# Kernel optimization log

Hardware: AMD Instinct MI355X
Metric: run time of the kernel (lower is better)

The kernel has to match this reference:

```python
import jax, jax.numpy as jnp
import numpy as np
from jax import lax

B, C, H, W = 4, 128, 64, 64
D = C // 2          # VSSBlock hidden_dim
DI = 2 * D          # SS2D d_inner (expand=2)
N = 16              # d_state
R = max(D // 16, 1) # dt_rank
K = 4               # scan directions

def dwconv(x, w, b):
    y = lax.conv_general_dilated(x, w, (1, 1), [(1, 1), (1, 1)],
        dimension_numbers=('NCHW', 'OIHW', 'NCHW'), feature_group_count=x.shape[1])
    return y + b[None, :, None, None]

def layer_norm(x, g, b, eps=1e-5):
    mu = jnp.mean(x, axis=-1, keepdims=True)
    var = jnp.var(x, axis=-1, keepdims=True)
    return (x - mu) * lax.rsqrt(var + eps) * g + b

def selective_scan(u, delta, A, Bs, Cs, Dp):
    # u, delta: (B,K,DI,L); Bs, Cs: (B,K,N,L); A: (K,DI,N); Dp: (K,DI)
    uT = jnp.moveaxis(u, -1, 0)
    dT = jnp.moveaxis(delta, -1, 0)
    BT = jnp.moveaxis(Bs, -1, 0)
    CT = jnp.moveaxis(Cs, -1, 0)
    h0 = jnp.zeros(u.shape[:3] + (A.shape[-1],), u.dtype)
    def step(h, inp):
        u_t, d_t, B_t, C_t = inp
        dA = jnp.exp(d_t[..., None] * A)                       # (B,K,DI,N)
        h = dA * h + (d_t * u_t)[..., None] * B_t[:, :, None, :]
        return h, jnp.einsum('bkdn,bkn->bkd', h, C_t)
    _, ys = lax.scan(step, h0, (uT, dT, BT, CT))
    return jnp.moveaxis(ys, 0, -1) + Dp[None, :, :, None] * u  # (B,K,DI,L)

def ss2d(x, in_proj_w, conv_w, conv_b, x_proj_w, dt_w, dt_b, A_logs, Ds, on_g, on_b, out_proj_w):
    # x: (B,H,W,D)
    b, h, w, _ = x.shape
    L = h * w
    xz = x @ in_proj_w.T                                       # (B,H,W,2*DI)
    xc, z = jnp.split(xz, 2, axis=-1)
    xc = jnp.transpose(xc, (0, 3, 1, 2))                       # (B,DI,H,W)
    xc = jax.nn.silu(dwconv(xc, conv_w, conv_b))
    x1 = xc.reshape(b, DI, L)                                  # row-major scan
    x2 = jnp.transpose(xc, (0, 1, 3, 2)).reshape(b, DI, L)     # col-major scan
    xs = jnp.stack([x1, x2, x1[:, :, ::-1], x2[:, :, ::-1]], axis=1)  # (B,K,DI,L)
    x_dbl = jnp.einsum('bkdl,kcd->bkcl', xs, x_proj_w)
    dts, Bsx, Csx = jnp.split(x_dbl, [R, R + N], axis=2)
    delta = jax.nn.softplus(jnp.einsum('bkrl,kdr->bkdl', dts, dt_w) + dt_b[None, :, :, None])
    A = -jnp.exp(A_logs).reshape(K, DI, N)
    out_y = selective_scan(xs, delta, A, Bsx, Csx, Ds.reshape(K, DI))  # (B,K,DI,L)
    inv_y = out_y[:, 2:4, :, ::-1]
    wh_y = jnp.transpose(out_y[:, 1].reshape(b, DI, w, h), (0, 1, 3, 2)).reshape(b, DI, L)
    invwh_y = jnp.transpose(inv_y[:, 1].reshape(b, DI, w, h), (0, 1, 3, 2)).reshape(b, DI, L)
    y = out_y[:, 0] + inv_y[:, 0] + wh_y + invwh_y             # (B,DI,L)
    y = jnp.transpose(y, (0, 2, 1)).reshape(b, h, w, DI)
    y = layer_norm(y, on_g, on_b) * jax.nn.silu(z)
    return y @ out_proj_w.T                                    # (B,H,W,D)

def _forward(x, dw_w, dw_b, scale, ln1_g, ln1_b, in_proj_w, conv_w, conv_b, x_proj_w, dt_w, dt_b, A_logs, Ds, out_norm_g, out_norm_b, out_proj_w, in_gamma, in_beta):
    xd = dwconv(x, dw_w, dw_b)
    x_1, x_2 = jnp.split(xd, 2, axis=1)
    def branch(xi):
        xp = jnp.transpose(xi, (0, 2, 3, 1))                   # (B,H,W,D)
        y = xp + ss2d(layer_norm(xp, ln1_g, ln1_b), in_proj_w, conv_w, conv_b,
                      x_proj_w, dt_w, dt_b, A_logs, Ds, out_norm_g, out_norm_b, out_proj_w)
        return scale * xi + jnp.transpose(y, (0, 3, 1, 2))
    xo = jnp.concatenate([branch(x_1), branch(x_2)], axis=1)
    mu = jnp.mean(xo, axis=(2, 3), keepdims=True)              # InstanceNorm2d(affine)
    var = jnp.var(xo, axis=(2, 3), keepdims=True)
    xo = (xo - mu) * lax.rsqrt(var + 1e-5) * in_gamma[None, :, None, None] + in_beta[None, :, None, None]
    return jnp.where(xo > 0, xo, 0.01 * xo)                    # LeakyReLU(0.01)

def setup_inputs():
    ks = jax.random.split(jax.random.key(0), 12)
    f = lambda k, shp, s=0.02: jax.random.normal(k, shp, jnp.float32) * s
    return dict(
        x=jax.random.normal(ks[0], (B, C, H, W), jnp.float32),
        dw_w=f(ks[1], (C, 1, 3, 3), 0.1), dw_b=f(ks[2], (C,), 0.1),
        scale=jnp.ones((1,), jnp.float32),
        ln1_g=jnp.ones((D,), jnp.float32), ln1_b=jnp.zeros((D,), jnp.float32),
        in_proj_w=f(ks[3], (2 * DI, D)),
        conv_w=f(ks[4], (DI, 1, 3, 3), 0.1), conv_b=f(ks[5], (DI,), 0.1),
        x_proj_w=f(ks[6], (K, R + 2 * N, DI)),
        dt_w=f(ks[7], (K, DI, R), 0.1), dt_b=f(ks[8], (K, DI), 0.1),
        A_logs=f(ks[9], (K * DI, N), 0.5), Ds=jnp.ones((K * DI,), jnp.float32),
        out_norm_g=jnp.ones((DI,), jnp.float32), out_norm_b=jnp.zeros((DI,), jnp.float32),
        out_proj_w=f(ks[10], (D, DI)),
        in_gamma=jnp.ones((C,), jnp.float32), in_beta=jnp.zeros((C,), jnp.float32),
    )

def reference(x, dw_w, dw_b, scale, ln1_g, ln1_b, in_proj_w, conv_w, conv_b, x_proj_w, dt_w, dt_b, A_logs, Ds, out_norm_g, out_norm_b, out_proj_w, in_gamma, in_beta):
    return _forward(x, dw_w, dw_b, scale, ln1_g, ln1_b, in_proj_w, conv_w, conv_b, x_proj_w, dt_w, dt_b, A_logs, Ds, out_norm_g, out_norm_b, out_proj_w, in_gamma, in_beta)
```

## Files before the change

### kernel.cpp

```cpp
#include <hip/hip_runtime.h>
#include <hip/hip_bf16.h>


__device__ __forceinline__ float LD(const void* p, size_t i, bool isb) {
  if (isb) {
    unsigned short u = ((const unsigned short*)p)[i];
    return __uint_as_float(((unsigned)u) << 16);
  }
  return ((const float*)p)[i];
}
__device__ __forceinline__ unsigned short f2bf(float f) {
  unsigned u = __float_as_uint(f);
  u = (u + 0x7FFFu + ((u >> 16) & 1u)) >> 16;
  return (unsigned short)u;
}
__device__ __forceinline__ float silu_(float x) { return x / (1.f + __expf(-x)); }
__device__ __forceinline__ float softplus_(float x) {
  return x > 20.f ? x : __logf(1.f + __expf(x));
}
#define EXP2R(x) __builtin_amdgcn_exp2f(x)

__global__ void kdet(const void* x, int* flag) {
  if (threadIdx.x == 0 && blockIdx.x == 0) {
    const unsigned short* xs = (const unsigned short*)x;
    int bad = 0;
    for (int i = 0; i < 64; ++i) {
      int e = (xs[2 * i] >> 7) & 0xFF;
      if (e > 150 || e < 100) bad++;
    }
    *flag = (bad >= 16) ? 0 : 1;
  }
}

__global__ __launch_bounds__(256) void k0_conv_ln(
    const void* x, const void* dww, const void* dwb, const void* lg, const void* lb,
    const int* __restrict__ flag,
    float* __restrict__ T1, float* __restrict__ T2)
{
  bool isb = (*flag != 0);
  int e = blockIdx.x >> 6, h = blockIdx.x & 63;
  int b = e & 3, br = e >> 2;
  int t = threadIdx.x;
  __shared__ float sIn[3][64][67];
  for (int idx = t; idx < 3 * 64; idx += 256) {
    int r = idx >> 6, d = idx & 63;
    sIn[r][d][0] = 0.f; sIn[r][d][65] = 0.f;
  }
  for (int idx = t; idx < 3 * 64 * 64; idx += 256) {
    int r = idx >> 12, rem = idx & 4095, d = rem >> 6, w = rem & 63;
    int hh = h + r - 1;
    float v = 0.f;
    if (hh >= 0 && hh < 64) v = LD(x, ((size_t)(b * 128 + br * 64 + d) * 64 + hh) * 64 + w, isb);
    sIn[r][d][1 + w] = v;
  }
  __syncthreads();
  int w = t >> 2, g = t & 3;
  float vals[16]; float psum = 0.f, psq = 0.f;
#pragma unroll
  for (int j = 0; j < 16; ++j) {
    int d = g * 16 + j, c = br * 64 + d;
    float s = LD(dwb, c, isb);
#pragma unroll
    for (int kh = 0; kh < 3; ++kh)
#pragma unroll
      for (int kw = 0; kw < 3; ++kw)
        s += LD(dww, c * 9 + kh * 3 + kw, isb) * sIn[kh][d][w + kw];
    vals[j] = s; psum += s; psq += s * s;
  }
  size_t base = ((size_t)e * 4096 + h * 64) * 64 + (size_t)t * 16;
#pragma unroll
  for (int j4 = 0; j4 < 4; ++j4) {
    float4 o; o.x = vals[j4*4]; o.y = vals[j4*4+1]; o.z = vals[j4*4+2]; o.w = vals[j4*4+3];
    *(float4*)(T1 + base + j4 * 4) = o;
  }
  __shared__ float sS[64][4], sQ[64][4];
  sS[w][g] = psum; sQ[w][g] = psq;
  __syncthreads();
  float m = (sS[w][0] + sS[w][1] + sS[w][2] + sS[w][3]) * (1.f / 64.f);
  float q = (sQ[w][0] + sQ[w][1] + sQ[w][2] + sQ[w][3]) * (1.f / 64.f);
  float rs = rsqrtf(q - m * m + 1e-5f);
#pragma unroll
  for (int j4 = 0; j4 < 4; ++j4) {
    float tmp[4];
#pragma unroll
    for (int jj = 0; jj < 4; ++jj) {
      int j = j4 * 4 + jj; int d = g * 16 + j;
      tmp[jj] = (vals[j] - m) * rs * LD(lg, d, isb) + LD(lb, d, isb);
    }
    float4 o; o.x = tmp[0]; o.y = tmp[1]; o.z = tmp[2]; o.w = tmp[3];
    *(float4*)(T2 + base + j4 * 4) = o;
  }
}

__global__ __launch_bounds__(256) void k2_inproj(
    const float* __restrict__ T2, const void* Wip, const int* __restrict__ flag,
    float* __restrict__ T3, float* __restrict__ T4)
{
  bool isb = (*flag != 0);
  int mt = blockIdx.x, ct = blockIdx.y;
  int t = threadIdx.x;
  __shared__ float sA[64][68];
  __shared__ float sB[64][68];
  int row0 = mt * 64;
  for (int q = t; q < 1024; q += 256) {
    int l = q >> 4, d4 = (q & 15) * 4;
    float4 v = *(const float4*)(T2 + (size_t)(row0 + l) * 64 + d4);
    sA[d4][l] = v.x; sA[d4+1][l] = v.y; sA[d4+2][l] = v.z; sA[d4+3][l] = v.w;
  }
  for (int q = t; q < 1024; q += 256) {
    int cl = q >> 4, d4 = (q & 15) * 4;
    size_t base = (size_t)(ct * 64 + cl) * 64 + d4;
    sB[d4][cl]   = LD(Wip, base, isb);
    sB[d4+1][cl] = LD(Wip, base + 1, isb);
    sB[d4+2][cl] = LD(Wip, base + 2, isb);
    sB[d4+3][cl] = LD(Wip, base + 3, isb);
  }
  __syncthreads();
  int ty = t >> 4, tx = t & 15;
  float acc[4][4];
#pragma unroll
  for (int i = 0; i < 4; ++i)
#pragma unroll
    for (int j = 0; j < 4; ++j) acc[i][j] = 0.f;
  for (int kk = 0; kk < 64; ++kk) {
    float4 a = *(const float4*)&sA[kk][ty * 4];
    float4 bq = *(const float4*)&sB[kk][tx * 4];
    float aa[4] = {a.x, a.y, a.z, a.w}, bb[4] = {bq.x, bq.y, bq.z, bq.w};
#pragma unroll
    for (int i = 0; i < 4; ++i)
#pragma unroll
      for (int j = 0; j < 4; ++j) acc[i][j] += aa[i] * bb[j];
  }
  int c0 = ct * 64 + tx * 4;
#pragma unroll
  for (int i = 0; i < 4; ++i) {
    size_t row = (size_t)row0 + ty * 4 + i;
    float4 o;
    if (c0 < 128) {
      o.x = acc[i][0]; o.y = acc[i][1]; o.z = acc[i][2]; o.w = acc[i][3];
      *(float4*)(T3 + row * 128 + c0) = o;
    } else {
      o.x = silu_(acc[i][0]); o.y = silu_(acc[i][1]); o.z = silu_(acc[i][2]); o.w = silu_(acc[i][3]);
      *(float4*)(T4 + row * 128 + (c0 - 128)) = o;
    }
  }
}

__global__ __launch_bounds__(256) void k3_conv2(
    const float* __restrict__ T3, const void* cw, const void* cb, const void* Ds,
    const int* __restrict__ flag,
    float* __restrict__ U0, float* __restrict__ U1, float* __restrict__ Ysum)
{
  bool isb = (*flag != 0);
  int e = blockIdx.x >> 6, h = blockIdx.x & 63, dc = blockIdx.y;
  int t = threadIdx.x;
  __shared__ float sI[3][66][65];
  for (int idx = t; idx < 3 * 2 * 64; idx += 256) {
    int r = idx / 128, rem = idx % 128, side = rem >> 6, d = rem & 63;
    sI[r][side * 65][d] = 0.f;
  }
  for (int idx = t; idx < 3 * 64 * 64; idx += 256) {
    int r = idx >> 12, rem = idx & 4095, w = rem >> 6, d = rem & 63;
    int hh = h + r - 1;
    float v = 0.f;
    if (hh >= 0 && hh < 64) v = T3[((size_t)e * 4096 + hh * 64 + w) * 128 + dc * 64 + d];
    sI[r][1 + w][d] = v;
  }
  __syncthreads();
  int d = t & 63, wq = t >> 6;
  int c2 = dc * 64 + d;
  float wt[9];
#pragma unroll
  for (int m = 0; m < 9; ++m) wt[m] = LD(cw, c2 * 9 + m, isb);
  float bias = LD(cb, c2, isb);
  float sd = LD(Ds, c2, isb) + LD(Ds, 128 + c2, isb) + LD(Ds, 256 + c2, isb) + LD(Ds, 384 + c2, isb);
  size_t eb = (size_t)e * 4096;
#pragma unroll
  for (int i = 0; i < 16; ++i) {
    int w = wq * 16 + i;
    float s = bias;
#pragma unroll
    for (int kh = 0; kh < 3; ++kh)
#pragma unroll
      for (int kw = 0; kw < 3; ++kw)
        s += wt[kh * 3 + kw] * sI[kh][w + kw][d];
    s = silu_(s);
    U0[(eb + h * 64 + w) * 128 + c2] = s;
    U1[(eb + w * 64 + h) * 128 + c2] = s;
    Ysum[(eb + h * 64 + w) * 128 + c2] = sd * s;
  }
}

__global__ __launch_bounds__(256) void k5_xdbl(
    const float* __restrict__ U0, const float* __restrict__ U1,
    const void* xpw, const int* __restrict__ flag,
    float* __restrict__ dts4, float* __restrict__ Bb2, float* __restrict__ Cb2)
{
  bool isb = (*flag != 0);
  int lt = blockIdx.x;
  int ek = blockIdx.y;
  int e = ek >> 2, k = ek & 3;
  int ls0 = lt * 64;
  int t = threadIdx.x;
  __shared__ float sU[64][132];
  __shared__ float sW[36][132];
  for (int idx = t; idx < 36 * 128; idx += 256) {
    int c = idx >> 7, d = idx & 127;
    sW[c][d] = LD(xpw, ((size_t)k * 36 + c) * 128 + d, isb);
  }
  const float* usrc = (k & 1) ? U1 : U0;
  bool rev = (k >= 2);
  for (int idx = t; idx < 2048; idx += 256) {
    int l = idx >> 5, d4 = (idx & 31) * 4;
    int row = rev ? (4095 - ls0 - l) : (ls0 + l);
    float4 v = *(const float4*)(usrc + ((size_t)e * 4096 + row) * 128 + d4);
    *(float4*)&sU[l][d4] = v;
  }
  __syncthreads();
  int l = t & 63, cg = t >> 6;
  float acc[9];
#pragma unroll
  for (int j = 0; j < 9; ++j) acc[j] = 0.f;
  for (int dd = 0; dd < 32; ++dd) {
    float4 u4 = *(const float4*)&sU[l][dd * 4];
    float ua[4] = {u4.x, u4.y, u4.z, u4.w};
#pragma unroll
    for (int j = 0; j < 9; ++j) {
      float4 w4 = *(const float4*)&sW[cg * 9 + j][dd * 4];
      acc[j] += ua[0] * w4.x + ua[1] * w4.y + ua[2] * w4.z + ua[3] * w4.w;
    }
  }
  size_t row = (size_t)ek * 4096 + ls0 + l;
  if (cg == 0) {
    float4 o; o.x = acc[0]; o.y = acc[1]; o.z = acc[2]; o.w = acc[3];
    *(float4*)(dts4 + row * 4) = o;
#pragma unroll
    for (int j = 4; j < 9; ++j) Bb2[row * 16 + (j - 4)] = acc[j];
  } else {
#pragma unroll
    for (int j = 0; j < 9; ++j) {
      int c = cg * 9 + j;
      if (c < 20) Bb2[row * 16 + (c - 4)] = acc[j];
      else Cb2[row * 16 + (c - 20)] = acc[j];
    }
  }
}

template<int NSTEPS>
__global__ __launch_bounds__(128) void k6a_chunk(
    const float* __restrict__ U0, const float* __restrict__ U1,
    const float* __restrict__ dts4, const float* __restrict__ Bb2,
    const void* alog, const void* dtw, const void* dtb, const int* __restrict__ flag,
    float* __restrict__ Hs)
{
  bool isb = (*flag != 0);
  int chunk = blockIdx.x, ek = blockIdx.y;
  int e = ek >> 2, k = ek & 3;
  int d = threadIdx.x;
  int ls0 = chunk * NSTEPS;
  float a2[16];
#pragma unroll
  for (int n = 0; n < 16; ++n)
    a2[n] = -__expf(LD(alog, ((size_t)k * 128 + d) * 16 + n, isb)) * 1.44269504f;
  float w0 = LD(dtw, ((size_t)k * 128 + d) * 4 + 0, isb);
  float w1 = LD(dtw, ((size_t)k * 128 + d) * 4 + 1, isb);
  float w2 = LD(dtw, ((size_t)k * 128 + d) * 4 + 2, isb);
  float w3 = LD(dtw, ((size_t)k * 128 + d) * 4 + 3, isb);
  float bd = LD(dtb, k * 128 + d, isb);
  float h[16];
#pragma unroll
  for (int n = 0; n < 16; ++n) h[n] = 0.f;
  float sdelta = 0.f;
  const float* usrc = (k & 1) ? U1 : U0;
  const bool rev = (k >= 2);
  const float* ubase = usrc + (size_t)e * 4096 * 128 + d;
  const float4* sbase = (const float4*)(dts4 + ((size_t)ek * 4096 + ls0) * 4);
  const float4* bbase = (const float4*)(Bb2 + ((size_t)ek * 4096 + ls0) * 16);
#pragma unroll 2
  for (int t = 0; t < NSTEPS; ++t) {
    float4 s4 = sbase[t];
    float xv = bd + w0 * s4.x + w1 * s4.y + w2 * s4.z + w3 * s4.w;
    float dlt = softplus_(xv);
    int urow = rev ? (4095 - ls0 - t) : (ls0 + t);
    float uu = ubase[(size_t)urow * 128];
    float du = dlt * uu;
    float4 b0 = bbase[t * 4 + 0], b1 = bbase[t * 4 + 1], b2 = bbase[t * 4 + 2], b3 = bbase[t * 4 + 3];
    float bb[16] = {b0.x,b0.y,b0.z,b0.w, b1.x,b1.y,b1.z,b1.w,
                    b2.x,b2.y,b2.z,b2.w, b3.x,b3.y,b3.z,b3.w};
    sdelta += dlt;
#pragma unroll
    for (int n = 0; n < 16; ++n) {
      float dA = EXP2R(dlt * a2[n]);
      h[n] = fmaf(dA, h[n], du * bb[n]);
    }
  }
  float2* hp = (float2*)Hs + ((size_t)chunk * 65536 + ek * 2048 + d * 16);
#pragma unroll
  for (int n = 0; n < 16; ++n) {
    float2 o; o.x = h[n]; o.y = EXP2R(a2[n] * sdelta);
    hp[n] = o;
  }
}

__global__ __launch_bounds__(256) void k6b_carry(
    float* __restrict__ Hs, int nchunks)
{
  int idx = blockIdx.x * 256 + threadIdx.x;
  float2* hs = (float2*)Hs;
  float carry = 0.f;
  for (int c = 0; c < nchunks; ++c) {
    float2 v = hs[(size_t)c * 65536 + idx];
    Hs[((size_t)c * 65536 + idx) * 2] = carry;
    carry = v.x + v.y * carry;
  }
}

template<int NSTEPS>
__global__ __launch_bounds__(128) void k6c_apply(
    const float* __restrict__ U0, const float* __restrict__ U1,
    float* __restrict__ Ysum, const float* __restrict__ dts4,
    const float* __restrict__ Bb2, const float* __restrict__ Cb2,
    const void* alog, const void* dtw, const void* dtb,
    const float* __restrict__ Hs, const int* __restrict__ flag)
{
  bool isb = (*flag != 0);
  int chunk = blockIdx.x, ek = blockIdx.y;
  int e = ek >> 2, k = ek & 3;
  int d = threadIdx.x;
  int ls0 = chunk * NSTEPS;
  float a2[16];
#pragma unroll
  for (int n = 0; n < 16; ++n)
    a2[n] = -__expf(LD(alog, ((size_t)k * 128 + d) * 16 + n, isb)) * 1.44269504f;
  float w0 = LD(dtw, ((size_t)k * 128 + d) * 4 + 0, isb);
  float w1 = LD(dtw, ((size_t)k * 128 + d) * 4 + 1, isb);
  float w2 = LD(dtw, ((size_t)k * 128 + d) * 4 + 2, isb);
  float w3 = LD(dtw, ((size_t)k * 128 + d) * 4 + 3, isb);
  float bd = LD(dtb, k * 128 + d, isb);
  float h[16];
  const float* hp = Hs + ((size_t)chunk * 65536 + ek * 2048 + d * 16) * 2;
#pragma unroll
  for (int n = 0; n < 16; ++n) h[n] = hp[2 * n];
  const float* usrc = (k & 1) ? U1 : U0;
  const bool rev = (k >= 2);
  float* ybase = Ysum + (size_t)e * 4096 * 128 + d;
  const float* ubase = usrc + (size_t)e * 4096 * 128 + d;
  const float4* sbase = (const float4*)(dts4 + ((size_t)ek * 4096 + ls0) * 4);
  const float4* bbase = (const float4*)(Bb2 + ((size_t)ek * 4096 + ls0) * 16);
  const float4* cbase = (const float4*)(Cb2 + ((size_t)ek * 4096 + ls0) * 16);
#pragma unroll 2
  for (int t = 0; t < NSTEPS; ++t) {
    float4 s4 = sbase[t];
    float xv = bd + w0 * s4.x + w1 * s4.y + w2 * s4.z + w3 * s4.w;
    float dlt = softplus_(xv);
    int urow = rev ? (4095 - ls0 - t) : (ls0 + t);
    float uu = ubase[(size_t)urow * 128];
    float du = dlt * uu;
    float4 b0 = bbase[t * 4 + 0], b1 = bbase[t * 4 + 1], b2 = bbase[t * 4 + 2], b3 = bbase[t * 4 + 3];
    float4 c0 = cbase[t * 4 + 0], c1 = cbase[t * 4 + 1], c2 = cbase[t * 4 + 2], c3 = cbase[t * 4 + 3];
    float bb[16] = {b0.x,b0.y,b0.z,b0.w, b1.x,b1.y,b1.z,b1.w,
                    b2.x,b2.y,b2.z,b2.w, b3.x,b3.y,b3.z,b3.w};
    float cc[16] = {c0.x,c0.y,c0.z,c0.w, c1.x,c1.y,c1.z,c1.w,
                    c2.x,c2.y,c2.z,c2.w, c3.x,c3.y,c3.z,c3.w};
    float ya = 0.f, yb = 0.f, yc = 0.f, yd = 0.f;
#pragma unroll
    for (int n = 0; n < 16; n += 4) {
      float dA0 = EXP2R(dlt * a2[n]);
      float dA1 = EXP2R(dlt * a2[n+1]);
      float dA2 = EXP2R(dlt * a2[n+2]);
      float dA3 = EXP2R(dlt * a2[n+3]);
      h[n]   = fmaf(dA0, h[n],   du * bb[n]);
      h[n+1] = fmaf(dA1, h[n+1], du * bb[n+1]);
      h[n+2] = fmaf(dA2, h[n+2], du * bb[n+2]);
      h[n+3] = fmaf(dA3, h[n+3], du * bb[n+3]);
      ya = fmaf(h[n],   cc[n],   ya);
      yb = fmaf(h[n+1], cc[n+1], yb);
      yc = fmaf(h[n+2], cc[n+2], yc);
      yd = fmaf(h[n+3], cc[n+3], yd);
    }
    int p = ls0 + t;
    int orow;
    if (k == 0)      orow = p;
    else if (k == 1) orow = ((p & 63) << 6) | (p >> 6);
    else if (k == 2) orow = 4095 - p;
    else { int q = 4095 - p; orow = ((q & 63) << 6) | (q >> 6); }
    atomicAdd(ybase + (size_t)orow * 128, (ya + yb) + (yc + yd));
  }
}

__global__ __launch_bounds__(256) void k7b_out(
    const float* __restrict__ Ysum, const float* __restrict__ T4,
    const float* __restrict__ T1,
    const void* ong, const void* onb, const void* opw, const void* scale_p,
    const int* __restrict__ flag,
    float* __restrict__ P)
{
  bool isb = (*flag != 0);
  int bid = blockIdx.x; int e = bid >> 7, lt = bid & 127;
  int l0 = lt * 32;
  int t = threadIdx.x;
  __shared__ float sY[32][132];
  __shared__ float sWo[64][132];
  __shared__ float sMu[32], sRs[32];
  __shared__ float sPs[32][8], sPq[32][8];
  __shared__ float sP[64][33];
  for (int idx = t; idx < 8192; idx += 256) sWo[idx >> 7][idx & 127] = LD(opw, idx, isb);
  for (int q = t; q < 1024; q += 256) {
    int l = q >> 5, d4 = (q & 31) * 4;
    float4 v = *(const float4*)(Ysum + ((size_t)e * 4096 + l0 + l) * 128 + d4);
    *(float4*)&sY[l][d4] = v;
  }
  __syncthreads();
  {
    int l = t & 31, g = t >> 5;
    float s = 0.f, q2 = 0.f;
#pragma unroll
    for (int j = 0; j < 16; ++j) { float v = sY[l][g * 16 + j]; s += v; q2 += v * v; }
    sPs[l][g] = s; sPq[l][g] = q2;
  }
  __syncthreads();
  if (t < 32) {
    float s = 0.f, q2 = 0.f;
#pragma unroll
    for (int g = 0; g < 8; ++g) { s += sPs[t][g]; q2 += sPq[t][g]; }
    float mu = s * (1.f / 128.f);
    float var = q2 * (1.f / 128.f) - mu * mu;
    sMu[t] = mu; sRs[t] = rsqrtf(var + 1e-5f);
  }
  __syncthreads();
  for (int idx = t; idx < 4096; idx += 256) {
    int l = idx >> 7, dd2 = idx & 127;
    float v = (sY[l][dd2] - sMu[l]) * sRs[l] * LD(ong, dd2, isb) + LD(onb, dd2, isb);
    v *= T4[((size_t)e * 4096 + l0 + l) * 128 + dd2];
    sY[l][dd2] = v;
  }
  __syncthreads();
  float ops = 1.f + LD(scale_p, 0, isb);
  {
    int l = t & 31, cg = t >> 5;
    float acc[8];
#pragma unroll
    for (int j = 0; j < 8; ++j) acc[j] = 0.f;
    for (int dd = 0; dd < 32; ++dd) {
      float4 v4 = *(const float4*)&sY[l][dd * 4];
      float va[4] = {v4.x, v4.y, v4.z, v4.w};
#pragma unroll
      for (int j = 0; j < 8; ++j) {
        float4 w4 = *(const float4*)&sWo[cg * 8 + j][dd * 4];
        acc[j] += va[0] * w4.x + va[1] * w4.y + va[2] * w4.z + va[3] * w4.w;
      }
    }
#pragma unroll
    for (int j = 0; j < 8; ++j) {
      int c = cg * 8 + j;
      sP[c][l] = acc[j] + ops * T1[((size_t)e * 4096 + l0 + l) * 64 + c];
    }
  }
  __syncthreads();
  for (int q = t; q < 512; q += 256) {
    int c = q >> 3, lq = (q & 7) * 4;
    float4 o; o.x = sP[c][lq]; o.y = sP[c][lq+1]; o.z = sP[c][lq+2]; o.w = sP[c][lq+3];
    *(float4*)(P + ((size_t)e * 64 + c) * 4096 + l0 + lq) = o;
  }
}

__global__ __launch_bounds__(256) void k7c_final(
    const float* __restrict__ P, const void* gamma, const void* beta,
    const int* __restrict__ flag, void* __restrict__ out)
{
  bool isb = (*flag != 0);
  int bid = blockIdx.x; int e = bid >> 6, c = bid & 63;
  int b = e & 3, br = e >> 2;
  int cg = br * 64 + c;
  int t = threadIdx.x;
  const float* p = P + ((size_t)e * 64 + c) * 4096;
  float s = 0.f, q2 = 0.f;
  for (int q = t; q < 1024; q += 256) {
    float4 v = *(const float4*)(p + q * 4);
    s += v.x + v.y + v.z + v.w;
    q2 += v.x * v.x + v.y * v.y + v.z * v.z + v.w * v.w;
  }
#pragma unroll
  for (int off = 1; off < 64; off <<= 1) { s += __shfl_xor(s, off); q2 += __shfl_xor(q2, off); }
  __shared__ float rS[4], rQ[4];
  if ((t & 63) == 0) { rS[t >> 6] = s; rQ[t >> 6] = q2; }
  __syncthreads();
  float ts = rS[0] + rS[1] + rS[2] + rS[3];
  float tq = rQ[0] + rQ[1] + rQ[2] + rQ[3];
  float mu = ts * (1.f / 4096.f);
  float var = tq * (1.f / 4096.f) - mu * mu;
  float rsg = rsqrtf(var + 1e-5f);
  float gm = LD(gamma, cg, isb), bt = LD(beta, cg, isb);
  size_t obase = ((size_t)(b * 128 + cg)) * 4096;
  for (int q = t; q < 1024; q += 256) {
    float4 v = *(const float4*)(p + q * 4);
    float o0 = (v.x - mu) * rsg * gm + bt; o0 = o0 > 0.f ? o0 : 0.01f * o0;
    float o1 = (v.y - mu) * rsg * gm + bt; o1 = o1 > 0.f ? o1 : 0.01f * o1;
    float o2 = (v.z - mu) * rsg * gm + bt; o2 = o2 > 0.f ? o2 : 0.01f * o2;
    float o3 = (v.w - mu) * rsg * gm + bt; o3 = o3 > 0.f ? o3 : 0.01f * o3;
    if (isb) {
      unsigned short* op = (unsigned short*)out + obase;
      unsigned lo = (unsigned)f2bf(o0) | ((unsigned)f2bf(o1) << 16);
      unsigned hi = (unsigned)f2bf(o2) | ((unsigned)f2bf(o3) << 16);
      uint2 u; u.x = lo; u.y = hi;
      *(uint2*)(op + q * 4) = u;
    } else {
      float* op = (float*)out + obase;
      float4 o; o.x = o0; o.y = o1; o.z = o2; o.w = o3;
      *(float4*)(op + q * 4) = o;
    }
  }
}

extern "C" void kernel_launch(void* const* d_in, const int* in_sizes, int n_in,
                              void* d_out, int out_size, void* d_ws, size_t ws_size,
                              hipStream_t stream) {
  (void)in_sizes; (void)n_in; (void)out_size;
  const void* x      = d_in[0];
  const void* dw_w   = d_in[1];
  const void* dw_b   = d_in[2];
  const void* scale  = d_in[3];
  const void* ln1_g  = d_in[4];
  const void* ln1_b  = d_in[5];
  const void* ipw    = d_in[6];
  const void* conv_w = d_in[7];
  const void* conv_b = d_in[8];
  const void* xpw    = d_in[9];
  const void* dtw    = d_in[10];
  const void* dtb    = d_in[11];
  const void* alog   = d_in[12];
  const void* Ds     = d_in[13];
  const void* ong    = d_in[14];
  const void* onb    = d_in[15];
  const void* opw    = d_in[16];
  const void* ing    = d_in[17];
  const void* inb    = d_in[18];

  float* ws = (float*)d_ws;
  float* T1  = ws;
  float* T2  = ws + 2097152;
  float* T3  = ws + 4194304;
  float* T4  = ws + 8388608;
  float* U0  = ws + 12582912;
  float* U1  = ws + 16777216;
  float* Ysum = ws + 20971520;
  float* Bb2 = T3;
  float* Cb2 = T3 + 2097152;
  float* Hs  = ws + 37748736;
  float* dts4 = T2;

  size_t base_f = 37748736;
  size_t need64 = (base_f + (size_t)64 * 65536 * 2 + 16) * 4;
  int nch = (ws_size >= need64) ? 64 : 32;
  int* flag = (int*)(ws + base_f + (size_t)nch * 65536 * 2);

  hipLaunchKernelGGL(kdet, dim3(1), dim3(64), 0, stream, x, flag);
  hipLaunchKernelGGL(k0_conv_ln, dim3(512), dim3(256), 0, stream, x, dw_w, dw_b, ln1_g, ln1_b, flag, T1, T2);
  hipLaunchKernelGGL(k2_inproj, dim3(512, 4), dim3(256), 0, stream, T2, ipw, flag, T3, T4);
  hipLaunchKernelGGL(k3_conv2, dim3(512, 2), dim3(256), 0, stream, T3, conv_w, conv_b, Ds, flag, U0, U1, Ysum);
  hipLaunchKernelGGL(k5_xdbl, dim3(64, 32), dim3(256), 0, stream, U0, U1, xpw, flag, dts4, Bb2, Cb2);
  if (nch == 64) {
    hipLaunchKernelGGL(k6a_chunk<64>, dim3(64, 32), dim3(128), 0, stream, U0, U1, dts4, Bb2, alog, dtw, dtb, flag, Hs);
    hipLaunchKernelGGL(k6b_carry, dim3(256), dim3(256), 0, stream, Hs, 64);
    hipLaunchKernelGGL(k6c_apply<64>, dim3(64, 32), dim3(128), 0, stream, U0, U1, Ysum, dts4, Bb2, Cb2, alog, dtw, dtb, Hs, flag);
  } else {
    hipLaunchKernelGGL(k6a_chunk<128>, dim3(32, 32), dim3(128), 0, stream, U0, U1, dts4, Bb2, alog, dtw, dtb, flag, Hs);
    hipLaunchKernelGGL(k6b_carry, dim3(256), dim3(256), 0, stream, Hs, 32);
    hipLaunchKernelGGL(k6c_apply<128>, dim3(32, 32), dim3(128), 0, stream, U0, U1, Ysum, dts4, Bb2, Cb2, alog, dtw, dtb, Hs, flag);
  }
  hipLaunchKernelGGL(k7b_out, dim3(1024), dim3(256), 0, stream, Ysum, T4, T1, ong, onb, opw, scale, flag, T2);
  hipLaunchKernelGGL(k7c_final, dim3(512), dim3(256), 0, stream, T2, ing, inb, flag, d_out);
}
```

Before: 460.8 us.

## Drop transposed U copy, split scan state, accumulate scan outputs in shared tiles

The conv kernel now writes only the row-major activation. The transposed and reversed views are formed by index remapping inside the x_proj and scan kernels. The chunked scan kernels split the 16 state dims across two thread halves, which doubles thread-level parallelism. The apply kernel pairs each forward direction with its reversed direction in one block so that both map to the same output rows, and accumulates y in shared memory with LDS atomics instead of global atomics. Row-major and column-major outputs go to separate buffers, the D skip term is folded in, and the final out-projection kernel sums the two buffers with a transposed read. This removes the U1 and Ysum writes plus the global atomics, at the cost of strided gather reads and an extra transposed load in k7b.

```diff
diff --git a/kernel.cpp b/kernel.cpp
--- a/kernel.cpp
+++ b/kernel.cpp
@@ -147,9 +147,9 @@
 }
 
 __global__ __launch_bounds__(256) void k3_conv2(
-    const float* __restrict__ T3, const void* cw, const void* cb, const void* Ds,
+    const float* __restrict__ T3, const void* cw, const void* cb,
     const int* __restrict__ flag,
-    float* __restrict__ U0, float* __restrict__ U1, float* __restrict__ Ysum)
+    float* __restrict__ U0)
 {
   bool isb = (*flag != 0);
   int e = blockIdx.x >> 6, h = blockIdx.x & 63, dc = blockIdx.y;
@@ -173,7 +173,6 @@
 #pragma unroll
   for (int m = 0; m < 9; ++m) wt[m] = LD(cw, c2 * 9 + m, isb);
   float bias = LD(cb, c2, isb);
-  float sd = LD(Ds, c2, isb) + LD(Ds, 128 + c2, isb) + LD(Ds, 256 + c2, isb) + LD(Ds, 384 + c2, isb);
   size_t eb = (size_t)e * 4096;
 #pragma unroll
   for (int i = 0; i < 16; ++i) {
@@ -186,13 +185,11 @@
         s += wt[kh * 3 + kw] * sI[kh][w + kw][d];
     s = silu_(s);
     U0[(eb + h * 64 + w) * 128 + c2] = s;
-    U1[(eb + w * 64 + h) * 128 + c2] = s;
-    Ysum[(eb + h * 64 + w) * 128 + c2] = sd * s;
   }
 }
 
 __global__ __launch_bounds__(256) void k5_xdbl(
-    const float* __restrict__ U0, const float* __restrict__ U1,
+    const float* __restrict__ U0,
     const void* xpw, const int* __restrict__ flag,
     float* __restrict__ dts4, float* __restrict__ Bb2, float* __restrict__ Cb2)
 {
@@ -208,12 +205,13 @@
     int c = idx >> 7, d = idx & 127;
     sW[c][d] = LD(xpw, ((size_t)k * 36 + c) * 128 + d, isb);
   }
-  const float* usrc = (k & 1) ? U1 : U0;
-  bool rev = (k >= 2);
+  const bool rev = (k >= 2);
+  const int trq = (k & 1);
   for (int idx = t; idx < 2048; idx += 256) {
     int l = idx >> 5, d4 = (idx & 31) * 4;
-    int row = rev ? (4095 - ls0 - l) : (ls0 + l);
-    float4 v = *(const float4*)(usrc + ((size_t)e * 4096 + row) * 128 + d4);
+    int p = rev ? (4095 - ls0 - l) : (ls0 + l);
+    int row = trq ? (((p & 63) << 6) | (p >> 6)) : p;
+    float4 v = *(const float4*)(U0 + ((size_t)e * 4096 + row) * 128 + d4);
     *(float4*)&sU[l][d4] = v;
   }
   __syncthreads();
@@ -247,8 +245,8 @@
 }
 
 template<int NSTEPS>
-__global__ __launch_bounds__(128) void k6a_chunk(
-    const float* __restrict__ U0, const float* __restrict__ U1,
+__global__ __launch_bounds__(256) void k6a_chunk(
+    const float* __restrict__ U0,
     const float* __restrict__ dts4, const float* __restrict__ Bb2,
     const void* alog, const void* dtw, const void* dtb, const int* __restrict__ flag,
     float* __restrict__ Hs)
@@ -256,47 +254,49 @@
   bool isb = (*flag != 0);
   int chunk = blockIdx.x, ek = blockIdx.y;
   int e = ek >> 2, k = ek & 3;
-  int d = threadIdx.x;
+  int t = threadIdx.x;
+  int d = t & 127, nh = t >> 7;
   int ls0 = chunk * NSTEPS;
-  float a2[16];
-#pragma unroll
-  for (int n = 0; n < 16; ++n)
-    a2[n] = -__expf(LD(alog, ((size_t)k * 128 + d) * 16 + n, isb)) * 1.44269504f;
+  float a2[8];
+#pragma unroll
+  for (int n = 0; n < 8; ++n)
+    a2[n] = -__expf(LD(alog, ((size_t)k * 128 + d) * 16 + nh * 8 + n, isb)) * 1.44269504f;
   float w0 = LD(dtw, ((size_t)k * 128 + d) * 4 + 0, isb);
   float w1 = LD(dtw, ((size_t)k * 128 + d) * 4 + 1, isb);
   float w2 = LD(dtw, ((size_t)k * 128 + d) * 4 + 2, isb);
   float w3 = LD(dtw, ((size_t)k * 128 + d) * 4 + 3, isb);
   float bd = LD(dtb, k * 128 + d, isb);
-  float h[16];
-#pragma unroll
-  for (int n = 0; n < 16; ++n) h[n] = 0.f;
+  float h[8];
+#pragma unroll
+  for (int n = 0; n < 8; ++n) h[n] = 0.f;
   float sdelta = 0.f;
-  const float* usrc = (k & 1) ? U1 : U0;
-  const bool rev = (k >= 2);
-  const float* ubase = usrc + (size_t)e * 4096 * 128 + d;
+  const bool rv = (k >= 2);
+  const int tq = (k & 1);
+  const float* ubase = U0 + (size_t)e * 4096 * 128 + d;
   const float4* sbase = (const float4*)(dts4 + ((size_t)ek * 4096 + ls0) * 4);
-  const float4* bbase = (const float4*)(Bb2 + ((size_t)ek * 4096 + ls0) * 16);
+  const float4* bbase = (const float4*)(Bb2 + ((size_t)ek * 4096 + ls0) * 16) + nh * 2;
 #pragma unroll 2
-  for (int t = 0; t < NSTEPS; ++t) {
-    float4 s4 = sbase[t];
+  for (int s = 0; s < NSTEPS; ++s) {
+    float4 s4 = sbase[s];
     float xv = bd + w0 * s4.x + w1 * s4.y + w2 * s4.z + w3 * s4.w;
     float dlt = softplus_(xv);
-    int urow = rev ? (4095 - ls0 - t) : (ls0 + t);
-    float uu = ubase[(size_t)urow * 128];
+    int p = ls0 + s;
+    int r0 = rv ? (4095 - p) : p;
+    int row = tq ? (((r0 & 63) << 6) | (r0 >> 6)) : r0;
+    float uu = ubase[(size_t)row * 128];
     float du = dlt * uu;
-    float4 b0 = bbase[t * 4 + 0], b1 = bbase[t * 4 + 1], b2 = bbase[t * 4 + 2], b3 = bbase[t * 4 + 3];
-    float bb[16] = {b0.x,b0.y,b0.z,b0.w, b1.x,b1.y,b1.z,b1.w,
-                    b2.x,b2.y,b2.z,b2.w, b3.x,b3.y,b3.z,b3.w};
+    float4 b0 = bbase[s * 4], b1 = bbase[s * 4 + 1];
+    float bb[8] = {b0.x, b0.y, b0.z, b0.w, b1.x, b1.y, b1.z, b1.w};
     sdelta += dlt;
 #pragma unroll
-    for (int n = 0; n < 16; ++n) {
+    for (int n = 0; n < 8; ++n) {
       float dA = EXP2R(dlt * a2[n]);
       h[n] = fmaf(dA, h[n], du * bb[n]);
     }
   }
-  float2* hp = (float2*)Hs + ((size_t)chunk * 65536 + ek * 2048 + d * 16);
-#pragma unroll
-  for (int n = 0; n < 16; ++n) {
+  float2* hp = (float2*)Hs + ((size_t)chunk * 65536 + ek * 2048 + d * 16 + nh * 8);
+#pragma unroll
+  for (int n = 0; n < 8; ++n) {
     float2 o; o.x = h[n]; o.y = EXP2R(a2[n] * sdelta);
     hp[n] = o;
   }
@@ -316,81 +316,84 @@
 }
 
 template<int NSTEPS>
-__global__ __launch_bounds__(128) void k6c_apply(
-    const float* __restrict__ U0, const float* __restrict__ U1,
-    float* __restrict__ Ysum, const float* __restrict__ dts4,
+__global__ __launch_bounds__(512) void k6c_apply(
+    const float* __restrict__ U0,
+    float* __restrict__ Ysum, float* __restrict__ YsumT,
+    const float* __restrict__ dts4,
     const float* __restrict__ Bb2, const float* __restrict__ Cb2,
-    const void* alog, const void* dtw, const void* dtb,
+    const void* alog, const void* dtw, const void* dtb, const void* Ds,
     const float* __restrict__ Hs, const int* __restrict__ flag)
 {
-  bool isb = (*flag != 0);
-  int chunk = blockIdx.x, ek = blockIdx.y;
-  int e = ek >> 2, k = ek & 3;
-  int d = threadIdx.x;
+  constexpr int NCH = 4096 / NSTEPS;
+  bool isb = (*flag != 0);
+  int c = blockIdx.x;
+  int e = blockIdx.y >> 1, pa = blockIdx.y & 1;
+  int t = threadIdx.x;
+  int d = t & 127, nh = (t >> 7) & 1, hf = t >> 8;
+  int k = hf ? (pa + 2) : pa;
+  int chunk = hf ? (NCH - 1 - c) : c;
+  int ek = e * 4 + k;
   int ls0 = chunk * NSTEPS;
-  float a2[16];
-#pragma unroll
-  for (int n = 0; n < 16; ++n)
-    a2[n] = -__expf(LD(alog, ((size_t)k * 128 + d) * 16 + n, isb)) * 1.44269504f;
+  __shared__ float ytile[NSTEPS][128];
+  for (int i = t; i < NSTEPS * 128; i += 512) ((float*)ytile)[i] = 0.f;
+  float a2[8];
+#pragma unroll
+  for (int n = 0; n < 8; ++n)
+    a2[n] = -__expf(LD(alog, ((size_t)k * 128 + d) * 16 + nh * 8 + n, isb)) * 1.44269504f;
   float w0 = LD(dtw, ((size_t)k * 128 + d) * 4 + 0, isb);
   float w1 = LD(dtw, ((size_t)k * 128 + d) * 4 + 1, isb);
   float w2 = LD(dtw, ((size_t)k * 128 + d) * 4 + 2, isb);
   float w3 = LD(dtw, ((size_t)k * 128 + d) * 4 + 3, isb);
   float bd = LD(dtb, k * 128 + d, isb);
-  float h[16];
-  const float* hp = Hs + ((size_t)chunk * 65536 + ek * 2048 + d * 16) * 2;
-#pragma unroll
-  for (int n = 0; n < 16; ++n) h[n] = hp[2 * n];
-  const float* usrc = (k & 1) ? U1 : U0;
-  const bool rev = (k >= 2);
-  float* ybase = Ysum + (size_t)e * 4096 * 128 + d;
-  const float* ubase = usrc + (size_t)e * 4096 * 128 + d;
+  float sd = 0.f;
+  if (pa == 0 && hf == 0 && nh == 0)
+    sd = LD(Ds, d, isb) + LD(Ds, 128 + d, isb) + LD(Ds, 256 + d, isb) + LD(Ds, 384 + d, isb);
+  float h[8];
+  const float* hp = Hs + ((size_t)chunk * 65536 + ek * 2048 + d * 16 + nh * 8) * 2;
+#pragma unroll
+  for (int n = 0; n < 8; ++n) h[n] = hp[2 * n];
+  const float* ubase = U0 + (size_t)e * 4096 * 128 + d;
   const float4* sbase = (const float4*)(dts4 + ((size_t)ek * 4096 + ls0) * 4);
-  const float4* bbase = (const float4*)(Bb2 + ((size_t)ek * 4096 + ls0) * 16);
-  const float4* cbase = (const float4*)(Cb2 + ((size_t)ek * 4096 + ls0) * 16);
+  const float4* bbase = (const float4*)(Bb2 + ((size_t)ek * 4096 + ls0) * 16) + nh * 2;
+  const float4* cbase = (const float4*)(Cb2 + ((size_t)ek * 4096 + ls0) * 16) + nh * 2;
+  __syncthreads();
 #pragma unroll 2
-  for (int t = 0; t < NSTEPS; ++t) {
-    float4 s4 = sbase[t];
+  for (int s = 0; s < NSTEPS; ++s) {
+    float4 s4 = sbase[s];
     float xv = bd + w0 * s4.x + w1 * s4.y + w2 * s4.z + w3 * s4.w;
     float dlt = softplus_(xv);
-    int urow = rev ? (4095 - ls0 - t) : (ls0 + t);
-    float uu = ubase[(size_t)urow * 128];
+    int p = ls0 + s;
+    int r0 = hf ? (4095 - p) : p;
+    int row = pa ? (((r0 & 63) << 6) | (r0 >> 6)) : r0;
+    float uu = ubase[(size_t)row * 128];
     float du = dlt * uu;
-    float4 b0 = bbase[t * 4 + 0], b1 = bbase[t * 4 + 1], b2 = bbase[t * 4 + 2], b3 = bbase[t * 4 + 3];
-    float4 c0 = cbase[t * 4 + 0], c1 = cbase[t * 4 + 1], c2 = cbase[t * 4 + 2], c3 = cbase[t * 4 + 3];
-    float bb[16] = {b0.x,b0.y,b0.z,b0.w, b1.x,b1.y,b1.z,b1.w,
-                    b2.x,b2.y,b2.z,b2.w, b3.x,b3.y,b3.z,b3.w};
-    float cc[16] = {c0.x,c0.y,c0.z,c0.w, c1.x,c1.y,c1.z,c1.w,
-                    c2.x,c2.y,c2.z,c2.w, c3.x,c3.y,c3.z,c3.w};
-    float ya = 0.f, yb = 0.f, yc = 0.f, yd = 0.f;
-#pragma unroll
-    for (int n = 0; n < 16; n += 4) {
-      float dA0 = EXP2R(dlt * a2[n]);
-      float dA1 = EXP2R(dlt * a2[n+1]);
-      float dA2 = EXP2R(dlt * a2[n+2]);
-      float dA3 = EXP2R(dlt * a2[n+3]);
-      h[n]   = fmaf(dA0, h[n],   du * bb[n]);
-      h[n+1] = fmaf(dA1, h[n+1], du * bb[n+1]);
-      h[n+2] = fmaf(dA2, h[n+2], du * bb[n+2]);
-      h[n+3] = fmaf(dA3, h[n+3], du * bb[n+3]);
-      ya = fmaf(h[n],   cc[n],   ya);
-      yb = fmaf(h[n+1], cc[n+1], yb);
-      yc = fmaf(h[n+2], cc[n+2], yc);
-      yd = fmaf(h[n+3], cc[n+3], yd);
-    }
-    int p = ls0 + t;
-    int orow;
-    if (k == 0)      orow = p;
-    else if (k == 1) orow = ((p & 63) << 6) | (p >> 6);
-    else if (k == 2) orow = 4095 - p;
-    else { int q = 4095 - p; orow = ((q & 63) << 6) | (q >> 6); }
-    atomicAdd(ybase + (size_t)orow * 128, (ya + yb) + (yc + yd));
+    float4 b0 = bbase[s * 4], b1 = bbase[s * 4 + 1];
+    float4 c0 = cbase[s * 4], c1 = cbase[s * 4 + 1];
+    float bb[8] = {b0.x, b0.y, b0.z, b0.w, b1.x, b1.y, b1.z, b1.w};
+    float cc[8] = {c0.x, c0.y, c0.z, c0.w, c1.x, c1.y, c1.z, c1.w};
+    float y = 0.f;
+#pragma unroll
+    for (int n = 0; n < 8; ++n) {
+      float dA = EXP2R(dlt * a2[n]);
+      h[n] = fmaf(dA, h[n], du * bb[n]);
+      y = fmaf(h[n], cc[n], y);
+    }
+    int r = hf ? (NSTEPS - 1 - s) : s;
+    atomicAdd(&ytile[r][d], fmaf(sd, uu, y));
+  }
+  __syncthreads();
+  float* obase = (pa ? YsumT : Ysum) + ((size_t)e * 4096 + c * NSTEPS) * 128;
+  for (int i = t; i < NSTEPS * 32; i += 512) {
+    int r = i >> 5, d4 = (i & 31) * 4;
+    float4 o;
+    o.x = ytile[r][d4]; o.y = ytile[r][d4 + 1]; o.z = ytile[r][d4 + 2]; o.w = ytile[r][d4 + 3];
+    *(float4*)(obase + (size_t)r * 128 + d4) = o;
   }
 }
 
 __global__ __launch_bounds__(256) void k7b_out(
-    const float* __restrict__ Ysum, const float* __restrict__ T4,
-    const float* __restrict__ T1,
+    const float* __restrict__ Ysum, const float* __restrict__ YsumT,
+    const float* __restrict__ T4, const float* __restrict__ T1,
     const void* ong, const void* onb, const void* opw, const void* scale_p,
     const int* __restrict__ flag,
     float* __restrict__ P)
@@ -405,9 +408,13 @@
   __shared__ float sPs[32][8], sPq[32][8];
   __shared__ float sP[64][33];
   for (int idx = t; idx < 8192; idx += 256) sWo[idx >> 7][idx & 127] = LD(opw, idx, isb);
+  int hh = l0 >> 6;
+  int w0_ = l0 & 63;
   for (int q = t; q < 1024; q += 256) {
     int l = q >> 5, d4 = (q & 31) * 4;
     float4 v = *(const float4*)(Ysum + ((size_t)e * 4096 + l0 + l) * 128 + d4);
+    float4 v2 = *(const float4*)(YsumT + ((size_t)e * 4096 + (w0_ + l) * 64 + hh) * 128 + d4);
+    v.x += v2.x; v.y += v2.y; v.z += v2.z; v.w += v2.w;
     *(float4*)&sY[l][d4] = v;
   }
   __syncthreads();
@@ -542,7 +549,7 @@
   float* T3  = ws + 4194304;
   float* T4  = ws + 8388608;
   float* U0  = ws + 12582912;
-  float* U1  = ws + 16777216;
+  float* YsT = ws + 16777216;
   float* Ysum = ws + 20971520;
   float* Bb2 = T3;
   float* Cb2 = T3 + 2097152;
@@ -557,17 +564,17 @@
   hipLaunchKernelGGL(kdet, dim3(1), dim3(64), 0, stream, x, flag);
   hipLaunchKernelGGL(k0_conv_ln, dim3(512), dim3(256), 0, stream, x, dw_w, dw_b, ln1_g, ln1_b, flag, T1, T2);
   hipLaunchKernelGGL(k2_inproj, dim3(512, 4), dim3(256), 0, stream, T2, ipw, flag, T3, T4);
-  hipLaunchKernelGGL(k3_conv2, dim3(512, 2), dim3(256), 0, stream, T3, conv_w, conv_b, Ds, flag, U0, U1, Ysum);
-  hipLaunchKernelGGL(k5_xdbl, dim3(64, 32), dim3(256), 0, stream, U0, U1, xpw, flag, dts4, Bb2, Cb2);
+  hipLaunchKernelGGL(k3_conv2, dim3(512, 2), dim3(256), 0, stream, T3, conv_w, conv_b, flag, U0);
+  hipLaunchKernelGGL(k5_xdbl, dim3(64, 32), dim3(256), 0, stream, U0, xpw, flag, dts4, Bb2, Cb2);
   if (nch == 64) {
-    hipLaunchKernelGGL(k6a_chunk<64>, dim3(64, 32), dim3(128), 0, stream, U0, U1, dts4, Bb2, alog, dtw, dtb, flag, Hs);
+    hipLaunchKernelGGL(k6a_chunk<64>, dim3(64, 32), dim3(256), 0, stream, U0, dts4, Bb2, alog, dtw, dtb, flag, Hs);
     hipLaunchKernelGGL(k6b_carry, dim3(256), dim3(256), 0, stream, Hs, 64);
-    hipLaunchKernelGGL(k6c_apply<64>, dim3(64, 32), dim3(128), 0, stream, U0, U1, Ysum, dts4, Bb2, Cb2, alog, dtw, dtb, Hs, flag);
+    hipLaunchKernelGGL(k6c_apply<64>, dim3(64, 16), dim3(512), 0, stream, U0, Ysum, YsT, dts4, Bb2, Cb2, alog, dtw, dtb, Ds, Hs, flag);
   } else {
-    hipLaunchKernelGGL(k6a_chunk<128>, dim3(32, 32), dim3(128), 0, stream, U0, U1, dts4, Bb2, alog, dtw, dtb, flag, Hs);
+    hipLaunchKernelGGL(k6a_chunk<128>, dim3(32, 32), dim3(256), 0, stream, U0, dts4, Bb2, alog, dtw, dtb, flag, Hs);
     hipLaunchKernelGGL(k6b_carry, dim3(256), dim3(256), 0, stream, Hs, 32);
-    hipLaunchKernelGGL(k6c_apply<128>, dim3(32, 32), dim3(128), 0, stream, U0, U1, Ysum, dts4, Bb2, Cb2, alog, dtw, dtb, Hs, flag);
-  }
-  hipLaunchKernelGGL(k7b_out, dim3(1024), dim3(256), 0, stream, Ysum, T4, T1, ong, onb, opw, scale, flag, T2);
+    hipLaunchKernelGGL(k6c_apply<128>, dim3(32, 16), dim3(512), 0, stream, U0, Ysum, YsT, dts4, Bb2, Cb2, alog, dtw, dtb, Ds, Hs, flag);
+  }
+  hipLaunchKernelGGL(k7b_out, dim3(1024), dim3(256), 0, stream, Ysum, YsT, T4, T1, ong, onb, opw, scale, flag, T2);
   hipLaunchKernelGGL(k7c_final, dim3(512), dim3(256), 0, stream, T2, ing, inb, flag, d_out);
 }
```

Result: slower. 582.8 us (+26.5%).

## Drop transposed U1 copy, index U0 transposed in place, use 128 scan chunks

Applied to the files above, without the earlier changes.

Removes the column-major duplicate U1 written by the conv kernel. The x_proj and scan kernels now compute transposed row indices directly into U0, which frees workspace. That space is reused so the chunked scan can split into 128 chunks of 32 steps, which raises parallelism in k6a and k6c. The carry kernel now batches 8 chunk loads before its serial updates. The trade-off is strided, less coalesced U0 reads for the transposed directions and a longer serial carry loop.

```diff
diff --git a/kernel.cpp b/kernel.cpp
--- a/kernel.cpp
+++ b/kernel.cpp
@@ -149,7 +149,7 @@
 __global__ __launch_bounds__(256) void k3_conv2(
     const float* __restrict__ T3, const void* cw, const void* cb, const void* Ds,
     const int* __restrict__ flag,
-    float* __restrict__ U0, float* __restrict__ U1, float* __restrict__ Ysum)
+    float* __restrict__ U0, float* __restrict__ Ysum)
 {
   bool isb = (*flag != 0);
   int e = blockIdx.x >> 6, h = blockIdx.x & 63, dc = blockIdx.y;
@@ -186,13 +186,12 @@
         s += wt[kh * 3 + kw] * sI[kh][w + kw][d];
     s = silu_(s);
     U0[(eb + h * 64 + w) * 128 + c2] = s;
-    U1[(eb + w * 64 + h) * 128 + c2] = s;
     Ysum[(eb + h * 64 + w) * 128 + c2] = sd * s;
   }
 }
 
 __global__ __launch_bounds__(256) void k5_xdbl(
-    const float* __restrict__ U0, const float* __restrict__ U1,
+    const float* __restrict__ U0,
     const void* xpw, const int* __restrict__ flag,
     float* __restrict__ dts4, float* __restrict__ Bb2, float* __restrict__ Cb2)
 {
@@ -208,12 +207,13 @@
     int c = idx >> 7, d = idx & 127;
     sW[c][d] = LD(xpw, ((size_t)k * 36 + c) * 128 + d, isb);
   }
-  const float* usrc = (k & 1) ? U1 : U0;
-  bool rev = (k >= 2);
+  const bool rev = (k >= 2);
+  const int trq = (k & 1);
   for (int idx = t; idx < 2048; idx += 256) {
     int l = idx >> 5, d4 = (idx & 31) * 4;
-    int row = rev ? (4095 - ls0 - l) : (ls0 + l);
-    float4 v = *(const float4*)(usrc + ((size_t)e * 4096 + row) * 128 + d4);
+    int p = rev ? (4095 - ls0 - l) : (ls0 + l);
+    int row = trq ? (((p & 63) << 6) | (p >> 6)) : p;
+    float4 v = *(const float4*)(U0 + ((size_t)e * 4096 + row) * 128 + d4);
     *(float4*)&sU[l][d4] = v;
   }
   __syncthreads();
@@ -248,7 +248,7 @@
 
 template<int NSTEPS>
 __global__ __launch_bounds__(128) void k6a_chunk(
-    const float* __restrict__ U0, const float* __restrict__ U1,
+    const float* __restrict__ U0,
     const float* __restrict__ dts4, const float* __restrict__ Bb2,
     const void* alog, const void* dtw, const void* dtb, const int* __restrict__ flag,
     float* __restrict__ Hs)
@@ -271,20 +271,22 @@
 #pragma unroll
   for (int n = 0; n < 16; ++n) h[n] = 0.f;
   float sdelta = 0.f;
-  const float* usrc = (k & 1) ? U1 : U0;
-  const bool rev = (k >= 2);
-  const float* ubase = usrc + (size_t)e * 4096 * 128 + d;
+  const bool rv = (k >= 2);
+  const int tq = (k & 1);
+  const float* ubase = U0 + (size_t)e * 4096 * 128 + d;
   const float4* sbase = (const float4*)(dts4 + ((size_t)ek * 4096 + ls0) * 4);
   const float4* bbase = (const float4*)(Bb2 + ((size_t)ek * 4096 + ls0) * 16);
 #pragma unroll 2
-  for (int t = 0; t < NSTEPS; ++t) {
-    float4 s4 = sbase[t];
+  for (int s = 0; s < NSTEPS; ++s) {
+    float4 s4 = sbase[s];
     float xv = bd + w0 * s4.x + w1 * s4.y + w2 * s4.z + w3 * s4.w;
     float dlt = softplus_(xv);
-    int urow = rev ? (4095 - ls0 - t) : (ls0 + t);
-    float uu = ubase[(size_t)urow * 128];
+    int p = ls0 + s;
+    int r0 = rv ? (4095 - p) : p;
+    int row = tq ? (((r0 & 63) << 6) | (r0 >> 6)) : r0;
+    float uu = ubase[(size_t)row * 128];
     float du = dlt * uu;
-    float4 b0 = bbase[t * 4 + 0], b1 = bbase[t * 4 + 1], b2 = bbase[t * 4 + 2], b3 = bbase[t * 4 + 3];
+    float4 b0 = bbase[s * 4 + 0], b1 = bbase[s * 4 + 1], b2 = bbase[s * 4 + 2], b3 = bbase[s * 4 + 3];
     float bb[16] = {b0.x,b0.y,b0.z,b0.w, b1.x,b1.y,b1.z,b1.w,
                     b2.x,b2.y,b2.z,b2.w, b3.x,b3.y,b3.z,b3.w};
     sdelta += dlt;
@@ -308,16 +310,21 @@
   int idx = blockIdx.x * 256 + threadIdx.x;
   float2* hs = (float2*)Hs;
   float carry = 0.f;
-  for (int c = 0; c < nchunks; ++c) {
-    float2 v = hs[(size_t)c * 65536 + idx];
-    Hs[((size_t)c * 65536 + idx) * 2] = carry;
-    carry = v.x + v.y * carry;
+  for (int c0 = 0; c0 < nchunks; c0 += 8) {
+    float2 v[8];
+#pragma unroll
+    for (int j = 0; j < 8; ++j) v[j] = hs[(size_t)(c0 + j) * 65536 + idx];
+#pragma unroll
+    for (int j = 0; j < 8; ++j) {
+      Hs[((size_t)(c0 + j) * 65536 + idx) * 2] = carry;
+      carry = v[j].x + v[j].y * carry;
+    }
   }
 }
 
 template<int NSTEPS>
 __global__ __launch_bounds__(128) void k6c_apply(
-    const float* __restrict__ U0, const float* __restrict__ U1,
+    const float* __restrict__ U0,
     float* __restrict__ Ysum, const float* __restrict__ dts4,
     const float* __restrict__ Bb2, const float* __restrict__ Cb2,
     const void* alog, const void* dtw, const void* dtb,
@@ -341,23 +348,25 @@
   const float* hp = Hs + ((size_t)chunk * 65536 + ek * 2048 + d * 16) * 2;
 #pragma unroll
   for (int n = 0; n < 16; ++n) h[n] = hp[2 * n];
-  const float* usrc = (k & 1) ? U1 : U0;
-  const bool rev = (k >= 2);
+  const bool rv = (k >= 2);
+  const int tq = (k & 1);
+  const float* ubase = U0 + (size_t)e * 4096 * 128 + d;
   float* ybase = Ysum + (size_t)e * 4096 * 128 + d;
-  const float* ubase = usrc + (size_t)e * 4096 * 128 + d;
   const float4* sbase = (const float4*)(dts4 + ((size_t)ek * 4096 + ls0) * 4);
   const float4* bbase = (const float4*)(Bb2 + ((size_t)ek * 4096 + ls0) * 16);
   const float4* cbase = (const float4*)(Cb2 + ((size_t)ek * 4096 + ls0) * 16);
 #pragma unroll 2
-  for (int t = 0; t < NSTEPS; ++t) {
-    float4 s4 = sbase[t];
+  for (int s = 0; s < NSTEPS; ++s) {
+    float4 s4 = sbase[s];
     float xv = bd + w0 * s4.x + w1 * s4.y + w2 * s4.z + w3 * s4.w;
     float dlt = softplus_(xv);
-    int urow = rev ? (4095 - ls0 - t) : (ls0 + t);
-    float uu = ubase[(size_t)urow * 128];
+    int p = ls0 + s;
+    int r0 = rv ? (4095 - p) : p;
+    int row = tq ? (((r0 & 63) << 6) | (r0 >> 6)) : r0;
+    float uu = ubase[(size_t)row * 128];
     float du = dlt * uu;
-    float4 b0 = bbase[t * 4 + 0], b1 = bbase[t * 4 + 1], b2 = bbase[t * 4 + 2], b3 = bbase[t * 4 + 3];
-    float4 c0 = cbase[t * 4 + 0], c1 = cbase[t * 4 + 1], c2 = cbase[t * 4 + 2], c3 = cbase[t * 4 + 3];
+    float4 b0 = bbase[s * 4 + 0], b1 = bbase[s * 4 + 1], b2 = bbase[s * 4 + 2], b3 = bbase[s * 4 + 3];
+    float4 c0 = cbase[s * 4 + 0], c1 = cbase[s * 4 + 1], c2 = cbase[s * 4 + 2], c3 = cbase[s * 4 + 3];
     float bb[16] = {b0.x,b0.y,b0.z,b0.w, b1.x,b1.y,b1.z,b1.w,
                     b2.x,b2.y,b2.z,b2.w, b3.x,b3.y,b3.z,b3.w};
     float cc[16] = {c0.x,c0.y,c0.z,c0.w, c1.x,c1.y,c1.z,c1.w,
@@ -378,13 +387,7 @@
       yc = fmaf(h[n+2], cc[n+2], yc);
       yd = fmaf(h[n+3], cc[n+3], yd);
     }
-    int p = ls0 + t;
-    int orow;
-    if (k == 0)      orow = p;
-    else if (k == 1) orow = ((p & 63) << 6) | (p >> 6);
-    else if (k == 2) orow = 4095 - p;
-    else { int q = 4095 - p; orow = ((q & 63) << 6) | (q >> 6); }
-    atomicAdd(ybase + (size_t)orow * 128, (ya + yb) + (yc + yd));
+    atomicAdd(ybase + (size_t)row * 128, (ya + yb) + (yc + yd));
   }
 }
 
@@ -515,7 +518,7 @@
 extern "C" void kernel_launch(void* const* d_in, const int* in_sizes, int n_in,
                               void* d_out, int out_size, void* d_ws, size_t ws_size,
                               hipStream_t stream) {
-  (void)in_sizes; (void)n_in; (void)out_size;
+  (void)in_sizes; (void)n_in; (void)out_size; (void)ws_size;
   const void* x      = d_in[0];
   const void* dw_w   = d_in[1];
   const void* dw_b   = d_in[2];
@@ -542,32 +545,21 @@
   float* T3  = ws + 4194304;
   float* T4  = ws + 8388608;
   float* U0  = ws + 12582912;
-  float* U1  = ws + 16777216;
-  float* Ysum = ws + 20971520;
+  float* Hs  = ws + 16777216;
+  float* Ysum = ws + 33554432;
   float* Bb2 = T3;
   float* Cb2 = T3 + 2097152;
-  float* Hs  = ws + 37748736;
   float* dts4 = T2;
-
-  size_t base_f = 37748736;
-  size_t need64 = (base_f + (size_t)64 * 65536 * 2 + 16) * 4;
-  int nch = (ws_size >= need64) ? 64 : 32;
-  int* flag = (int*)(ws + base_f + (size_t)nch * 65536 * 2);
+  int* flag = (int*)(ws + 37748736);
 
   hipLaunchKernelGGL(kdet, dim3(1), dim3(64), 0, stream, x, flag);
   hipLaunchKernelGGL(k0_conv_ln, dim3(512), dim3(256), 0, stream, x, dw_w, dw_b, ln1_g, ln1_b, flag, T1, T2);
   hipLaunchKernelGGL(k2_inproj, dim3(512, 4), dim3(256), 0, stream, T2, ipw, flag, T3, T4);
-  hipLaunchKernelGGL(k3_conv2, dim3(512, 2), dim3(256), 0, stream, T3, conv_w, conv_b, Ds, flag, U0, U1, Ysum);
-  hipLaunchKernelGGL(k5_xdbl, dim3(64, 32), dim3(256), 0, stream, U0, U1, xpw, flag, dts4, Bb2, Cb2);
-  if (nch == 64) {
-    hipLaunchKernelGGL(k6a_chunk<64>, dim3(64, 32), dim3(128), 0, stream, U0, U1, dts4, Bb2, alog, dtw, dtb, flag, Hs);
-    hipLaunchKernelGGL(k6b_carry, dim3(256), dim3(256), 0, stream, Hs, 64);
-    hipLaunchKernelGGL(k6c_apply<64>, dim3(64, 32), dim3(128), 0, stream, U0, U1, Ysum, dts4, Bb2, Cb2, alog, dtw, dtb, Hs, flag);
-  } else {
-    hipLaunchKernelGGL(k6a_chunk<128>, dim3(32, 32), dim3(128), 0, stream, U0, U1, dts4, Bb2, alog, dtw, dtb, flag, Hs);
-    hipLaunchKernelGGL(k6b_carry, dim3(256), dim3(256), 0, stream, Hs, 32);
-    hipLaunchKernelGGL(k6c_apply<128>, dim3(32, 32), dim3(128), 0, stream, U0, U1, Ysum, dts4, Bb2, Cb2, alog, dtw, dtb, Hs, flag);
-  }
+  hipLaunchKernelGGL(k3_conv2, dim3(512, 2), dim3(256), 0, stream, T3, conv_w, conv_b, Ds, flag, U0, Ysum);
+  hipLaunchKernelGGL(k5_xdbl, dim3(64, 32), dim3(256), 0, stream, U0, xpw, flag, dts4, Bb2, Cb2);
+  hipLaunchKernelGGL(k6a_chunk<32>, dim3(128, 32), dim3(128), 0, stream, U0, dts4, Bb2, alog, dtw, dtb, flag, Hs);
+  hipLaunchKernelGGL(k6b_carry, dim3(256), dim3(256), 0, stream, Hs, 128);
+  hipLaunchKernelGGL(k6c_apply<32>, dim3(128, 32), dim3(128), 0, stream, U0, Ysum, dts4, Bb2, Cb2, alog, dtw, dtb, Hs, flag);
   hipLaunchKernelGGL(k7b_out, dim3(1024), dim3(256), 0, stream, Ysum, T4, T1, ong, onb, opw, scale, flag, T2);
   hipLaunchKernelGGL(k7c_final, dim3(512), dim3(256), 0, stream, T2, ing, inb, flag, d_out);
 }
```

Result: no change. 465.7 us (+1.0%).
